# Kernel tuning notes

Hardware: AMD Instinct MI355X
Metric: run time of the kernel (lower is better)

Reference implementation:

```python
import jax, jax.numpy as jnp
import numpy as np

N_NODES = 50000
N_EDGES = 800000
HIDDEN = 128
MSG = 128


def setup_inputs() -> dict:
    key = jax.random.key(0)
    ks = jax.random.split(key, 10)
    s = 0.05
    return {
        "x": jax.random.normal(ks[0], (N_NODES, HIDDEN), jnp.float32),
        "h": jax.random.normal(ks[1], (N_NODES, HIDDEN), jnp.float32),
        "src": jax.random.randint(ks[2], (N_EDGES,), 0, N_NODES, jnp.int32),
        "dst": jax.random.randint(ks[3], (N_EDGES,), 0, N_NODES, jnp.int32),
        "W_msg": s * jax.random.normal(ks[4], (MSG, 2 * HIDDEN), jnp.float32),
        "b_msg": s * jax.random.normal(ks[5], (MSG,), jnp.float32),
        "W_ih": s * jax.random.normal(ks[6], (3 * HIDDEN, HIDDEN + MSG), jnp.float32),
        "W_hh": s * jax.random.normal(ks[7], (3 * HIDDEN, HIDDEN), jnp.float32),
        "b_ih": s * jax.random.normal(ks[8], (3 * HIDDEN,), jnp.float32),
        "b_hh": s * jax.random.normal(ks[9], (3 * HIDDEN,), jnp.float32),
    }


def reference(x, h, src, dst, W_msg, b_msg, W_ih, W_hh, b_ih, b_hh):
    N = x.shape[0]
    # --- message: linear on concat(x_src, detached h_src) -> [E, MSG]
    h_det = jax.lax.stop_gradient(h)  # h.detach() in original
    feat = jnp.concatenate([x[src], h_det[src]], axis=1)  # [E, 2H]
    m = feat @ W_msg.T + b_msg  # [E, MSG]
    # --- mean aggregation over incoming edges; isolated nodes get zeros (DGL semantics)
    msum = jax.ops.segment_sum(m, dst, num_segments=N)  # [N, MSG]
    deg = jax.ops.segment_sum(jnp.ones((src.shape[0],), m.dtype), dst, num_segments=N)
    c = msum / jnp.maximum(deg, 1.0)[:, None]
    # --- GRUCell update (PyTorch GRUCell math)
    inp = jnp.concatenate([x, c], axis=1)  # [N, H+MSG]
    gi = inp @ W_ih.T + b_ih
    gh = h @ W_hh.T + b_hh
    i_r, i_z, i_n = jnp.split(gi, 3, axis=1)
    h_r, h_z, h_n = jnp.split(gh, 3, axis=1)
    r = jax.nn.sigmoid(i_r + h_r)
    z = jax.nn.sigmoid(i_z + h_z)
    n = jnp.tanh(i_n + r * h_n)
    return (1.0 - z) * n + z * h
```

## Files before the change

### kernel.cpp

```cpp
#include <hip/hip_runtime.h>

#define H 128
#define CAP 5120

typedef __attribute__((ext_vector_type(8))) short s16x8;
typedef __attribute__((ext_vector_type(2))) float f32x2;
typedef __attribute__((ext_vector_type(4))) float f32x4;

#define WAITBAR(N) asm volatile("s_waitcnt vmcnt(" #N ")\n\ts_barrier" ::: "memory")
#define BARO() asm volatile("s_barrier" ::: "memory")

__device__ __forceinline__ float bf2f(unsigned short u){
  unsigned x = ((unsigned)u) << 16;
  return __builtin_bit_cast(float, x);
}
__device__ __forceinline__ unsigned short f2bf(float f){
  unsigned u = __builtin_bit_cast(unsigned, f);
  u += 0x7fff + ((u >> 16) & 1);
  return (unsigned short)(u >> 16);
}

typedef __attribute__((address_space(1))) void gvoid;
typedef __attribute__((address_space(3))) void lvoid;
__device__ __forceinline__ void gload16(const void* g, void* l){
  __builtin_amdgcn_global_load_lds((gvoid*)(void*)g, (lvoid*)l, 16, 0, 0);
}

__global__ void pcfs_kernel(const float* x_, const float* h, const int* src, const int* dst,
                            const float* W_msg, const float* W_ih, const float* W_hh,
                            const float* b_ih, const float* b_hh,
                            unsigned short* xhs, unsigned char* xq,
                            unsigned* bucketArr, int* bucketCnt,
                            unsigned short* WmsgT, unsigned short* WbigT, float* biasb,
                            int NB, int YE, int nv, int E){
  int blk = blockIdx.x, tid = threadIdx.x;
  if(blk < YE){
    __shared__ int hcnt[256];
    __shared__ int hpos[256];
    hcnt[tid] = 0;
    __syncthreads();
    int base = blk*2048;
    unsigned pk[8]; int bk[8];
    #pragma unroll
    for(int it=0; it<8; ++it){
      int e = base + it*256 + tid;
      bk[it] = -1;
      if(e < E){
        int d = dst[e], s = src[e];
        pk[it] = ((unsigned)d << 16) | (unsigned)s;
        int b = d >> 8;
        bk[it] = b;
        atomicAdd(&hcnt[b], 1);
      }
    }
    __syncthreads();
    if(tid < NB){
      int c = hcnt[tid];
      hpos[tid] = (c > 0) ? atomicAdd(&bucketCnt[tid*32], c) : 0;
    }
    __syncthreads();
    #pragma unroll
    for(int it=0; it<8; ++it){
      if(bk[it] >= 0){
        int p = atomicAdd(&hpos[bk[it]], 1);
        if(p < CAP) bucketArr[(long)bk[it]*CAP + p] = pk[it];
      }
    }
    return;
  }
  long w0 = (long)(blk - YE)*2048 + tid;
  const int NW = 512*384;
  #pragma unroll 1
  for(int it=0; it<8; ++it){
    long w = w0 + (long)it*256;
    if(w < 2L*nv){
      const float* sp; long j; int add;
      if(w < nv){ sp = x_; j = w; add = 0; }
      else { sp = h; j = w - nv; add = 128; }
      float4 v = ((const float4*)sp)[j];
      ushort4 o; o.x=f2bf(v.x); o.y=f2bf(v.y); o.z=f2bf(v.z); o.w=f2bf(v.w);
      int node = (int)(j >> 5), col = add + ((int)j & 31)*4;
      int k = col >> 5, wc = col & 31;
      *(ushort4*)(xhs + (long)k*nv + node*32 + wc) = o;
      int r = __builtin_amdgcn_cvt_pk_fp8_f32(v.x, v.y, 0, false);
      r = __builtin_amdgcn_cvt_pk_fp8_f32(v.z, v.w, r, true);
      *(unsigned int*)(xq + (long)k*nv + node*32 + wc) = (unsigned)r;
      continue;
    }
    long i = w - 2L*nv;
    if(i < NW){
      int hf = (int)(i / 98304); int r1 = (int)(i % 98304);
      int kt = r1 / 16384; int r2 = r1 % 16384;
      int row = r2 / 64;   int r3 = r2 % 64;
      int cw = r3 >> 3;    int j = r3 & 7;
      int c = cw ^ (row & 7);
      int k = kt*64 + c*8 + j;
      int rp = hf*256 + row;
      int q = rp >> 2, g = rp & 3;
      float v;
      if(g < 3){
        int orow = g*128 + q;
        v = (k < 256) ? W_ih[orow*256 + k] : W_hh[orow*128 + (k-256)];
      } else {
        v = (k < 256) ? 0.f : W_hh[(256 + q)*128 + (k-256)];
      }
      WbigT[i] = f2bf(v);
    } else if(i < NW + 128*256){
      int j2 = (int)(i - NW);
      int kt = j2 / 8192; int r2 = j2 % 8192;
      int row = r2 / 64;  int r3 = r2 % 64;
      int cw = r3 >> 3;   int j = r3 & 7;
      int c = cw ^ (row & 7);
      int k = kt*64 + c*8 + j;
      WmsgT[j2] = f2bf(W_msg[row*256 + k]);
    } else if(i < NW + 128*256 + 512){
      int r = (int)(i - NW - 128*256);
      int q = r >> 2, g = r & 3;
      biasb[r] = (g < 3) ? (b_ih[g*128+q] + b_hh[g*128+q]) : b_hh[256+q];
    }
  }
}

__global__ void fill2_kernel(const unsigned* bucketArr, const int* bucketCnt,
                             int* rc, unsigned short* ss16, int N){
  __shared__ int lcnt[256];
  int b = blockIdx.x, tid = threadIdx.x;
  lcnt[tid] = 0;
  __syncthreads();
  int cnt = bucketCnt[b*32]; if(cnt > CAP) cnt = CAP;
  int nbase = b << 8;
  const unsigned* arr = bucketArr + (long)b*CAP;
  for(int i = tid; i < cnt; i += 256){
    unsigned e = arr[i];
    int d = e >> 16, s = e & 0xffff;
    int p = atomicAdd(&lcnt[d - nbase], 1);
    if(p < 128) ss16[((long)d << 7) + p] = (unsigned short)s;
  }
  __syncthreads();
  int node = nbase + tid;
  if(node < N) rc[node] = lcnt[tid];
}

__global__ void agg_kernel(const unsigned char* xq, const int* rc, const unsigned short* ss16,
                           unsigned short* Sb, int N){
  int tid = threadIdx.x;
  int group = tid >> 2, sub = tid & 3;
  int node = blockIdx.y*64 + group;
  if(node >= N) return;
  const unsigned char* base = xq + (long)blockIdx.x*(long)N*32;
  int cnt = rc[node];
  int use = (cnt < 128) ? cnt : 128;
  const long e0 = (long)node << 7;
  int co = sub*8;
  float a[8] = {0.f,0.f,0.f,0.f,0.f,0.f,0.f,0.f};
  int i = 0;
  for(; i+3 < use; i += 4){
    ushort4 idx = *(const ushort4*)(ss16 + e0 + i);
    uint2 q0 = *(const uint2*)(base + (long)idx.x*32 + co);
    uint2 q1 = *(const uint2*)(base + (long)idx.y*32 + co);
    uint2 q2 = *(const uint2*)(base + (long)idx.z*32 + co);
    uint2 q3 = *(const uint2*)(base + (long)idx.w*32 + co);
    #define ACC8(q) { \
      f32x2 l0 = __builtin_amdgcn_cvt_pk_f32_fp8((q).x, false); \
      f32x2 h0 = __builtin_amdgcn_cvt_pk_f32_fp8((q).x, true);  \
      f32x2 l1 = __builtin_amdgcn_cvt_pk_f32_fp8((q).y, false); \
      f32x2 h1 = __builtin_amdgcn_cvt_pk_f32_fp8((q).y, true);  \
      a[0]+=l0[0]; a[1]+=l0[1]; a[2]+=h0[0]; a[3]+=h0[1]; \
      a[4]+=l1[0]; a[5]+=l1[1]; a[6]+=h1[0]; a[7]+=h1[1]; }
    ACC8(q0); ACC8(q1); ACC8(q2); ACC8(q3);
  }
  for(; i < use; ++i){
    int s0 = ss16[e0 + i];
    uint2 q0 = *(const uint2*)(base + (long)s0*32 + co);
    ACC8(q0);
  }
  #undef ACC8
  float inv = (cnt > 0) ? 1.0f/(float)cnt : 0.f;
  unsigned short o[8];
  #pragma unroll
  for(int j=0;j<8;++j) o[j] = f2bf(a[j]*inv);
  *(s16x8*)(Sb + (long)node*256 + blockIdx.x*32 + co) = *(const s16x8*)o;
}

__global__ __launch_bounds__(512, 2) void fused_kernel(
    const unsigned short* xhs, const unsigned short* Sb,
    const unsigned short* WmsgT, const unsigned short* WbigT,
    const float* b_msg, const float* biasb, const int* deg,
    float* outp, int NN){
  __shared__ __align__(16) char lds[131072];
  char* W0 = lds;
  char* W1 = lds + 32768;
  char* N0 = lds + 65536;
  char* N1 = lds + 81920;
  char* ldsC = lds + 98304;
  float* ldsO = (float*)(lds + 32768);

  int tid = threadIdx.x;
  int lane = tid & 63, wv = tid >> 6;
  int l15 = lane & 15, l4 = lane >> 4;
  long nodebase = (long)blockIdx.x * 128;
  const long NV = (long)NN * 32;
  const f32x4 fz = {0.f,0.f,0.f,0.f};

  auto stageS = [&](int koff, char* dst){
    #pragma unroll
    for(int it=0; it<2; ++it){
      int slot = it*512 + tid;
      int row = slot >> 3, cw = slot & 7;
      int c = cw ^ (row & 7);
      long gr = nodebase + row; if(gr > NN-1) gr = NN-1;
      gload16(Sb + gr*256 + koff + c*8, dst + it*8192 + wv*1024);
    }
  };
  auto stageX = [&](int koff, char* dst){
    #pragma unroll
    for(int it=0; it<2; ++it){
      int slot = it*512 + tid;
      int row = slot >> 3, cw = slot & 7;
      int c = cw ^ (row & 7);
      int col = koff + c*8;
      int k = col >> 5, wc = col & 31;
      long gr = nodebase + row; if(gr > NN-1) gr = NN-1;
      gload16(xhs + (long)k*NV + gr*32 + wc, dst + it*8192 + wv*1024);
    }
  };
  auto stageW1k = [&](int kt, char* dst){
    #pragma unroll
    for(int it=0; it<2; ++it){
      int slot = it*512 + tid;
      gload16(WmsgT + kt*8192 + slot*8, dst + it*8192 + wv*1024);
    }
  };
  auto stageW3k = [&](int idx, char* dst){
    #pragma unroll
    for(int it=0; it<4; ++it){
      int slot = it*512 + tid;
      gload16(WbigT + (long)idx*16384 + slot*8, dst + it*8192 + wv*1024);
    }
  };

  int wm1 = wv >> 2, wn1 = wv & 3;
  f32x4 acc1[4][2];
  #pragma unroll
  for(int m=0;m<4;++m){ acc1[m][0]=fz; acc1[m][1]=fz; }

  auto compute1 = [&](const char* Wb, const char* Nb){
    __builtin_amdgcn_s_setprio(1);
    #pragma unroll
    for(int kk=0; kk<2; ++kk){
      s16x8 af[4], bn[2];
      #pragma unroll
      for(int m=0;m<4;++m){
        int fr = wm1*64 + m*16 + l15;
        af[m] = *(const s16x8*)(Wb + fr*128 + (((kk*4+l4) ^ (fr&7))*16));
      }
      #pragma unroll
      for(int n=0;n<2;++n){
        int nr = wn1*32 + n*16 + l15;
        bn[n] = *(const s16x8*)(Nb + nr*128 + (((kk*4+l4) ^ (nr&7))*16));
      }
      #pragma unroll
      for(int m=0;m<4;++m)
        #pragma unroll
        for(int n=0;n<2;++n)
          acc1[m][n] = __builtin_amdgcn_mfma_f32_16x16x32_bf16(af[m], bn[n], acc1[m][n], 0, 0, 0);
    }
    __builtin_amdgcn_s_setprio(0);
  };

  stageW1k(0, W0); stageS(0, N0);
  stageW1k(1, W1); stageS(64, N1);
  WAITBAR(4); compute1(W0, N0); BARO();
  stageW1k(2, W0); stageS(128, N0);
  WAITBAR(4); compute1(W1, N1); BARO();
  stageW1k(3, W1); stageS(192, N1);
  WAITBAR(4); compute1(W0, N0); BARO();
  stageW3k(0, W0); stageX(0, N0);
  WAITBAR(6); compute1(W1, N1); BARO();

  #pragma unroll
  for(int n=0;n<2;++n){
    int node_l = wn1*32 + n*16 + l15;
    long gn = nodebase + node_l; if(gn > NN-1) gn = NN-1;
    int dg = deg[gn];
    float msk = (dg > 0) ? 1.f : 0.f;
    #pragma unroll
    for(int m=0;m<4;++m){
      int ccb = wm1*64 + m*16 + l4*4;
      float4 bm = *(const float4*)(b_msg + ccb);
      ushort4 o;
      o.x = f2bf((acc1[m][n][0] + bm.x)*msk);
      o.y = f2bf((acc1[m][n][1] + bm.y)*msk);
      o.z = f2bf((acc1[m][n][2] + bm.z)*msk);
      o.w = f2bf((acc1[m][n][3] + bm.w)*msk);
      *(ushort4*)(ldsC + node_l*256 + (((ccb>>3) ^ (node_l&7))*16) + (ccb&4)*2) = o;
    }
  }
  __syncthreads();

  int wm = wv >> 1, wn = wv & 1;

  auto runHalf = [&](int hf){
    f32x4 acc3[4][4];
    #pragma unroll
    for(int m=0;m<4;++m)
      #pragma unroll
      for(int n=0;n<4;++n) acc3[m][n] = fz;

    auto computeN = [&](const char* Wb, const char* Nb){
      __builtin_amdgcn_s_setprio(1);
      #pragma unroll
      for(int kk=0; kk<2; ++kk){
        s16x8 af[4], bn[4];
        #pragma unroll
        for(int m=0;m<4;++m){
          int fr = wm*64 + m*16 + l15;
          af[m] = *(const s16x8*)(Wb + fr*128 + (((kk*4+l4) ^ (fr&7))*16));
        }
        #pragma unroll
        for(int n=0;n<4;++n){
          int nr = wn*64 + n*16 + l15;
          bn[n] = *(const s16x8*)(Nb + nr*128 + (((kk*4+l4) ^ (nr&7))*16));
        }
        #pragma unroll
        for(int m=0;m<4;++m)
          #pragma unroll
          for(int n=0;n<4;++n)
            acc3[m][n] = __builtin_amdgcn_mfma_f32_16x16x32_bf16(af[m], bn[n], acc3[m][n], 0, 0, 0);
      }
      __builtin_amdgcn_s_setprio(0);
    };
    auto computeC = [&](const char* Wb, int ktc){
      __builtin_amdgcn_s_setprio(1);
      #pragma unroll
      for(int kk=0; kk<2; ++kk){
        s16x8 af[4], bn[4];
        #pragma unroll
        for(int m=0;m<4;++m){
          int fr = wm*64 + m*16 + l15;
          af[m] = *(const s16x8*)(Wb + fr*128 + (((kk*4+l4) ^ (fr&7))*16));
        }
        #pragma unroll
        for(int n=0;n<4;++n){
          int nr = wn*64 + n*16 + l15;
          bn[n] = *(const s16x8*)(ldsC + nr*256 + (((ktc*8 + kk*4 + l4) ^ (nr&7))*16));
        }
        #pragma unroll
        for(int m=0;m<4;++m)
          #pragma unroll
          for(int n=0;n<4;++n)
            acc3[m][n] = __builtin_amdgcn_mfma_f32_16x16x32_bf16(af[m], bn[n], acc3[m][n], 0, 0, 0);
      }
      __builtin_amdgcn_s_setprio(0);
    };

    if(hf == 1) stageX(0, N0);
    stageW3k(hf*6+1, W1); stageX(64, N1);
    WAITBAR(6); computeN(W0, N0); BARO();
    stageW3k(hf*6+2, W0);
    WAITBAR(4); computeN(W1, N1); BARO();
    stageW3k(hf*6+3, W1);
    WAITBAR(4); computeC(W0, 0); BARO();
    stageW3k(hf*6+4, W0); stageX(128, N0);
    WAITBAR(6); computeC(W1, 1); BARO();
    stageW3k(hf*6+5, W1); stageX(192, N1);
    WAITBAR(6); computeN(W0, N0); BARO();
    if(hf == 0){
      stageW3k(6, W0);
      WAITBAR(4); computeN(W1, N1); BARO();
    } else {
      WAITBAR(0); computeN(W1, N1); BARO();
    }

    const char* hbuf = (hf == 0) ? N0 : N1;
    #pragma unroll
    for(int m=0;m<4;++m){
      int q = hf*64 + wm*16 + m*4 + l4;
      int ql = q & 63;
      float4 bb = *(const float4*)(biasb + q*4);
      #pragma unroll
      for(int n=0;n<4;++n){
        int node_l = wn*64 + n*16 + l15;
        unsigned short hu = *(const unsigned short*)(hbuf + node_l*128 +
                              (((ql>>3) ^ (node_l&7))*16) + (ql&7)*2);
        float hv = bf2f(hu);
        float vr  = acc3[m][n][0] + bb.x;
        float vz  = acc3[m][n][1] + bb.y;
        float vsn = acc3[m][n][2] + bb.z;
        float vhn = acc3[m][n][3] + bb.w;
        float r = 1.f/(1.f + __expf(-vr));
        float z = 1.f/(1.f + __expf(-vz));
        float narg = vsn + (r - 1.f)*vhn;
        float nn2 = 2.f/(1.f + __expf(-2.f*narg)) - 1.f;
        ldsO[node_l*64 + ql] = (1.f - z)*nn2 + z*hv;
      }
    }
    __syncthreads();

    #pragma unroll
    for(int it=0; it<4; ++it){
      int slot = it*512 + tid;
      int node_l = slot >> 4, f4 = slot & 15;
      long gn = nodebase + node_l;
      if(gn < NN){
        float4 v = *(const float4*)(ldsO + node_l*64 + f4*4);
        *(float4*)(outp + gn*128 + hf*64 + f4*4) = v;
      }
    }
    __syncthreads();
  };

  runHalf(0);
  runHalf(1);
}

extern "C" void kernel_launch(void* const* d_in, const int* in_sizes, int n_in,
                              void* d_out, int out_size, void* d_ws, size_t ws_size,
                              hipStream_t stream){
  const float* x     = (const float*)d_in[0];
  const float* h     = (const float*)d_in[1];
  const int*   src   = (const int*)d_in[2];
  const int*   dst   = (const int*)d_in[3];
  const float* W_msg = (const float*)d_in[4];
  const float* b_msg = (const float*)d_in[5];
  const float* W_ih  = (const float*)d_in[6];
  const float* W_hh  = (const float*)d_in[7];
  const float* b_ih  = (const float*)d_in[8];
  const float* b_hh  = (const float*)d_in[9];
  const int N = in_sizes[0] / H;
  const int E = in_sizes[2];
  float* out = (float*)d_out;

  char* p = (char*)d_ws;
  auto alloc = [&](size_t bytes)->char*{
    char* r = p; p += (bytes + 255) & ~(size_t)255; return r;
  };
  unsigned short* xhs   = (unsigned short*)alloc((size_t)N*256*2);
  unsigned short* Sb    = (unsigned short*)alloc((size_t)N*256*2);
  unsigned char*  xq    = (unsigned char*)alloc((size_t)N*256);
  unsigned short* WmsgT = (unsigned short*)alloc(128*256*2);
  unsigned short* WbigT = (unsigned short*)alloc(512*384*2);
  float*          biasb = (float*)alloc(512*4);
  int*            rc    = (int*)alloc((size_t)N*4);
  unsigned short* ss16  = (unsigned short*)alloc((size_t)N*128*2);
  int NB = (N + 255) >> 8;
  unsigned*       bktA  = (unsigned*)alloc((size_t)NB*CAP*4);
  int*            bktC  = (int*)alloc((size_t)NB*32*4);

  hipMemsetAsync(bktC, 0, (size_t)NB*32*4, stream);
  int nv = N*H/4;
  const int NPREP = 512*384 + 128*256 + 512;
  int YE = (E + 2047)/2048;
  long convTotal = 2L*nv + NPREP;
  int YC = (int)((convTotal + 2047)/2048);
  pcfs_kernel<<<YE + YC, 256, 0, stream>>>(
      x, h, src, dst, W_msg, W_ih, W_hh, b_ih, b_hh,
      xhs, xq, bktA, bktC, WmsgT, WbigT, biasb, NB, YE, nv, E);

  fill2_kernel<<<NB, 256, 0, stream>>>(bktA, bktC, rc, ss16, N);

  dim3 gagg(8, (N + 63)/64);
  agg_kernel<<<gagg, 256, 0, stream>>>(xq, rc, ss16, Sb, N);

  int nblk = (N + 127)/128;
  fused_kernel<<<nblk, 512, 0, stream>>>(
      xhs, Sb, WmsgT, WbigT, b_msg, biasb, rc, out, N);
}
```

Before: 130.7 us.

## Fold message linear into GRU input weights, removing first GEMM stage

```diff
diff --git a/kernel.cpp b/kernel.cpp
--- a/kernel.cpp
+++ b/kernel.cpp
@@ -27,11 +27,12 @@
 }
 
 __global__ void pcfs_kernel(const float* x_, const float* h, const int* src, const int* dst,
-                            const float* W_msg, const float* W_ih, const float* W_hh,
+                            const float* W_msg, const float* b_msg,
+                            const float* W_ih, const float* W_hh,
                             const float* b_ih, const float* b_hh,
                             unsigned short* xhs, unsigned char* xq,
                             unsigned* bucketArr, int* bucketCnt,
-                            unsigned short* WmsgT, unsigned short* WbigT, float* biasb,
+                            unsigned short* WbigT, float* biasb, float* bcv,
                             int NB, int YE, int nv, int E){
   int blk = blockIdx.x, tid = threadIdx.x;
   if(blk < YE){
@@ -69,7 +70,7 @@
     return;
   }
   long w0 = (long)(blk - YE)*2048 + tid;
-  const int NW = 512*384;
+  const int NW = 512*512;
   #pragma unroll 1
   for(int it=0; it<8; ++it){
     long w = w0 + (long)it*256;
@@ -89,34 +90,43 @@
     }
     long i = w - 2L*nv;
     if(i < NW){
-      int hf = (int)(i / 98304); int r1 = (int)(i % 98304);
-      int kt = r1 / 16384; int r2 = r1 % 16384;
-      int row = r2 / 64;   int r3 = r2 % 64;
-      int cw = r3 >> 3;    int j = r3 & 7;
+      int hf = (int)(i >> 17);  int r1 = (int)(i & 131071);
+      int kt = r1 >> 14;        int r2 = r1 & 16383;
+      int row = r2 >> 6;        int r3 = r2 & 63;
+      int cw = r3 >> 3;         int j = r3 & 7;
       int c = cw ^ (row & 7);
       int k = kt*64 + c*8 + j;
       int rp = hf*256 + row;
       int q = rp >> 2, g = rp & 3;
       float v;
+      if(g == 3){
+        v = (k >= 384) ? W_hh[(256+q)*128 + (k-384)] : 0.f;
+      } else {
+        int orow = g*128 + q;
+        if(k < 128) v = W_ih[orow*256 + k];
+        else if(k < 384){
+          int s = k - 128;
+          float acc = 0.f;
+          for(int m2 = 0; m2 < 128; ++m2)
+            acc += W_ih[orow*256 + 128 + m2] * W_msg[m2*256 + s];
+          v = acc;
+        } else v = W_hh[orow*128 + (k-384)];
+      }
+      WbigT[i] = f2bf(v);
+    } else if(i < NW + 512){
+      int r = (int)(i - NW);
+      int q = r >> 2, g = r & 3;
+      biasb[r] = (g < 3) ? (b_ih[g*128+q] + b_hh[g*128+q]) : b_hh[256+q];
+    } else if(i < NW + 1024){
+      int r = (int)(i - NW - 512);
+      int q = r >> 2, g = r & 3;
+      float acc = 0.f;
       if(g < 3){
         int orow = g*128 + q;
-        v = (k < 256) ? W_ih[orow*256 + k] : W_hh[orow*128 + (k-256)];
-      } else {
-        v = (k < 256) ? 0.f : W_hh[(256 + q)*128 + (k-256)];
-      }
-      WbigT[i] = f2bf(v);
-    } else if(i < NW + 128*256){
-      int j2 = (int)(i - NW);
-      int kt = j2 / 8192; int r2 = j2 % 8192;
-      int row = r2 / 64;  int r3 = r2 % 64;
-      int cw = r3 >> 3;   int j = r3 & 7;
-      int c = cw ^ (row & 7);
-      int k = kt*64 + c*8 + j;
-      WmsgT[j2] = f2bf(W_msg[row*256 + k]);
-    } else if(i < NW + 128*256 + 512){
-      int r = (int)(i - NW - 128*256);
-      int q = r >> 2, g = r & 3;
-      biasb[r] = (g < 3) ? (b_ih[g*128+q] + b_hh[g*128+q]) : b_hh[256+q];
+        for(int m2 = 0; m2 < 128; ++m2)
+          acc += W_ih[orow*256 + 128 + m2] * b_msg[m2];
+      }
+      bcv[r] = acc;
     }
   }
 }
@@ -184,15 +194,13 @@
 
 __global__ __launch_bounds__(512, 2) void fused_kernel(
     const unsigned short* xhs, const unsigned short* Sb,
-    const unsigned short* WmsgT, const unsigned short* WbigT,
-    const float* b_msg, const float* biasb, const int* deg,
-    float* outp, int NN){
-  __shared__ __align__(16) char lds[131072];
+    const unsigned short* WbigT, const float* biasb, const float* bcv,
+    const int* deg, float* outp, int NN){
+  __shared__ __align__(16) char lds[98304];
   char* W0 = lds;
   char* W1 = lds + 32768;
   char* N0 = lds + 65536;
   char* N1 = lds + 81920;
-  char* ldsC = lds + 98304;
   float* ldsO = (float*)(lds + 32768);
 
   int tid = threadIdx.x;
@@ -224,14 +232,12 @@
       gload16(xhs + (long)k*NV + gr*32 + wc, dst + it*8192 + wv*1024);
     }
   };
-  auto stageW1k = [&](int kt, char* dst){
-    #pragma unroll
-    for(int it=0; it<2; ++it){
-      int slot = it*512 + tid;
-      gload16(WmsgT + kt*8192 + slot*8, dst + it*8192 + wv*1024);
-    }
+  auto stageK = [&](int kt, char* dst){
+    if(kt < 2) stageX(kt*64, dst);
+    else if(kt < 6) stageS((kt-2)*64, dst);
+    else stageX(128 + (kt-6)*64, dst);
   };
-  auto stageW3k = [&](int idx, char* dst){
+  auto stageW = [&](int idx, char* dst){
     #pragma unroll
     for(int it=0; it<4; ++it){
       int slot = it*512 + tid;
@@ -239,75 +245,19 @@
     }
   };
 
-  int wm1 = wv >> 2, wn1 = wv & 3;
-  f32x4 acc1[4][2];
-  #pragma unroll
-  for(int m=0;m<4;++m){ acc1[m][0]=fz; acc1[m][1]=fz; }
-
-  auto compute1 = [&](const char* Wb, const char* Nb){
-    __builtin_amdgcn_s_setprio(1);
-    #pragma unroll
-    for(int kk=0; kk<2; ++kk){
-      s16x8 af[4], bn[2];
-      #pragma unroll
-      for(int m=0;m<4;++m){
-        int fr = wm1*64 + m*16 + l15;
-        af[m] = *(const s16x8*)(Wb + fr*128 + (((kk*4+l4) ^ (fr&7))*16));
-      }
-      #pragma unroll
-      for(int n=0;n<2;++n){
-        int nr = wn1*32 + n*16 + l15;
-        bn[n] = *(const s16x8*)(Nb + nr*128 + (((kk*4+l4) ^ (nr&7))*16));
-      }
-      #pragma unroll
-      for(int m=0;m<4;++m)
-        #pragma unroll
-        for(int n=0;n<2;++n)
-          acc1[m][n] = __builtin_amdgcn_mfma_f32_16x16x32_bf16(af[m], bn[n], acc1[m][n], 0, 0, 0);
-    }
-    __builtin_amdgcn_s_setprio(0);
-  };
-
-  stageW1k(0, W0); stageS(0, N0);
-  stageW1k(1, W1); stageS(64, N1);
-  WAITBAR(4); compute1(W0, N0); BARO();
-  stageW1k(2, W0); stageS(128, N0);
-  WAITBAR(4); compute1(W1, N1); BARO();
-  stageW1k(3, W1); stageS(192, N1);
-  WAITBAR(4); compute1(W0, N0); BARO();
-  stageW3k(0, W0); stageX(0, N0);
-  WAITBAR(6); compute1(W1, N1); BARO();
-
-  #pragma unroll
-  for(int n=0;n<2;++n){
-    int node_l = wn1*32 + n*16 + l15;
-    long gn = nodebase + node_l; if(gn > NN-1) gn = NN-1;
-    int dg = deg[gn];
-    float msk = (dg > 0) ? 1.f : 0.f;
-    #pragma unroll
-    for(int m=0;m<4;++m){
-      int ccb = wm1*64 + m*16 + l4*4;
-      float4 bm = *(const float4*)(b_msg + ccb);
-      ushort4 o;
-      o.x = f2bf((acc1[m][n][0] + bm.x)*msk);
-      o.y = f2bf((acc1[m][n][1] + bm.y)*msk);
-      o.z = f2bf((acc1[m][n][2] + bm.z)*msk);
-      o.w = f2bf((acc1[m][n][3] + bm.w)*msk);
-      *(ushort4*)(ldsC + node_l*256 + (((ccb>>3) ^ (node_l&7))*16) + (ccb&4)*2) = o;
-    }
-  }
-  __syncthreads();
-
   int wm = wv >> 1, wn = wv & 1;
 
-  auto runHalf = [&](int hf){
+  stageW(0, W0); stageK(0, N0);
+
+  #pragma unroll 1
+  for(int hf=0; hf<2; ++hf){
     f32x4 acc3[4][4];
     #pragma unroll
     for(int m=0;m<4;++m)
       #pragma unroll
       for(int n=0;n<4;++n) acc3[m][n] = fz;
 
-    auto computeN = [&](const char* Wb, const char* Nb){
+    auto compute = [&](const char* Wb, const char* Nb){
       __builtin_amdgcn_s_setprio(1);
       #pragma unroll
       for(int kk=0; kk<2; ++kk){
@@ -330,88 +280,70 @@
       }
       __builtin_amdgcn_s_setprio(0);
     };
-    auto computeC = [&](const char* Wb, int ktc){
-      __builtin_amdgcn_s_setprio(1);
-      #pragma unroll
-      for(int kk=0; kk<2; ++kk){
-        s16x8 af[4], bn[4];
-        #pragma unroll
-        for(int m=0;m<4;++m){
-          int fr = wm*64 + m*16 + l15;
-          af[m] = *(const s16x8*)(Wb + fr*128 + (((kk*4+l4) ^ (fr&7))*16));
-        }
-        #pragma unroll
-        for(int n=0;n<4;++n){
-          int nr = wn*64 + n*16 + l15;
-          bn[n] = *(const s16x8*)(ldsC + nr*256 + (((ktc*8 + kk*4 + l4) ^ (nr&7))*16));
-        }
-        #pragma unroll
-        for(int m=0;m<4;++m)
-          #pragma unroll
-          for(int n=0;n<4;++n)
-            acc3[m][n] = __builtin_amdgcn_mfma_f32_16x16x32_bf16(af[m], bn[n], acc3[m][n], 0, 0, 0);
-      }
-      __builtin_amdgcn_s_setprio(0);
-    };
-
-    if(hf == 1) stageX(0, N0);
-    stageW3k(hf*6+1, W1); stageX(64, N1);
-    WAITBAR(6); computeN(W0, N0); BARO();
-    stageW3k(hf*6+2, W0);
-    WAITBAR(4); computeN(W1, N1); BARO();
-    stageW3k(hf*6+3, W1);
-    WAITBAR(4); computeC(W0, 0); BARO();
-    stageW3k(hf*6+4, W0); stageX(128, N0);
-    WAITBAR(6); computeC(W1, 1); BARO();
-    stageW3k(hf*6+5, W1); stageX(192, N1);
-    WAITBAR(6); computeN(W0, N0); BARO();
-    if(hf == 0){
-      stageW3k(6, W0);
-      WAITBAR(4); computeN(W1, N1); BARO();
-    } else {
-      WAITBAR(0); computeN(W1, N1); BARO();
+
+    if(hf == 1) stageK(0, N0);
+    #pragma unroll
+    for(int kt=0; kt<8; ++kt){
+      char* cw_ = (kt&1) ? W1 : W0;
+      char* cn_ = (kt&1) ? N1 : N0;
+      char* nw_ = (kt&1) ? W0 : W1;
+      char* nn_ = (kt&1) ? N0 : N1;
+      if(kt < 7){
+        stageW(hf*8 + kt + 1, nw_); stageK(kt + 1, nn_);
+        WAITBAR(6);
+      } else if(hf == 0){
+        stageW(8, W0);
+        WAITBAR(4);
+      } else {
+        WAITBAR(0);
+      }
+      compute(cw_, cn_);
+      BARO();
     }
 
     const char* hbuf = (hf == 0) ? N0 : N1;
+    float mk[4];
+    #pragma unroll
+    for(int n=0;n<4;++n){
+      long gn = nodebase + wn*64 + n*16 + l15; if(gn > NN-1) gn = NN-1;
+      mk[n] = (deg[gn] > 0) ? 1.f : 0.f;
+    }
     #pragma unroll
     for(int m=0;m<4;++m){
       int q = hf*64 + wm*16 + m*4 + l4;
       int ql = q & 63;
-      float4 bb = *(const float4*)(biasb + q*4);
+      float4 bb  = *(const float4*)(biasb + q*4);
+      float4 bcq = *(const float4*)(bcv + q*4);
       #pragma unroll
       for(int n=0;n<4;++n){
         int node_l = wn*64 + n*16 + l15;
         unsigned short hu = *(const unsigned short*)(hbuf + node_l*128 +
                               (((ql>>3) ^ (node_l&7))*16) + (ql&7)*2);
         float hv = bf2f(hu);
-        float vr  = acc3[m][n][0] + bb.x;
-        float vz  = acc3[m][n][1] + bb.y;
-        float vsn = acc3[m][n][2] + bb.z;
-        float vhn = acc3[m][n][3] + bb.w;
+        float vr  = acc3[m][n][0] + bb.x + mk[n]*bcq.x;
+        float vz  = acc3[m][n][1] + bb.y + mk[n]*bcq.y;
+        float vsn = acc3[m][n][2] + bb.z + mk[n]*bcq.z;
+        float vhn = acc3[m][n][3] + bb.w + mk[n]*bcq.w;
         float r = 1.f/(1.f + __expf(-vr));
         float z = 1.f/(1.f + __expf(-vz));
         float narg = vsn + (r - 1.f)*vhn;
         float nn2 = 2.f/(1.f + __expf(-2.f*narg)) - 1.f;
-        ldsO[node_l*64 + ql] = (1.f - z)*nn2 + z*hv;
+        ldsO[node_l*64 + (ql ^ ((node_l & 15) << 2))] = (1.f - z)*nn2 + z*hv;
       }
     }
     __syncthreads();
-
     #pragma unroll
     for(int it=0; it<4; ++it){
       int slot = it*512 + tid;
       int node_l = slot >> 4, f4 = slot & 15;
       long gn = nodebase + node_l;
       if(gn < NN){
-        float4 v = *(const float4*)(ldsO + node_l*64 + f4*4);
+        float4 v = *(const float4*)(ldsO + node_l*64 + (((f4*4) ^ ((node_l & 15) << 2))));
         *(float4*)(outp + gn*128 + hf*64 + f4*4) = v;
       }
     }
     __syncthreads();
-  };
-
-  runHalf(0);
-  runHalf(1);
+  }
 }
 
 extern "C" void kernel_launch(void* const* d_in, const int* in_sizes, int n_in,
@@ -438,9 +370,9 @@
   unsigned short* xhs   = (unsigned short*)alloc((size_t)N*256*2);
   unsigned short* Sb    = (unsigned short*)alloc((size_t)N*256*2);
   unsigned char*  xq    = (unsigned char*)alloc((size_t)N*256);
-  unsigned short* WmsgT = (unsigned short*)alloc(128*256*2);
-  unsigned short* WbigT = (unsigned short*)alloc(512*384*2);
+  unsigned short* WbigT = (unsigned short*)alloc(512*512*2);
   float*          biasb = (float*)alloc(512*4);
+  float*          bcv   = (float*)alloc(512*4);
   int*            rc    = (int*)alloc((size_t)N*4);
   unsigned short* ss16  = (unsigned short*)alloc((size_t)N*128*2);
   int NB = (N + 255) >> 8;
@@ -449,13 +381,13 @@
 
   hipMemsetAsync(bktC, 0, (size_t)NB*32*4, stream);
   int nv = N*H/4;
-  const int NPREP = 512*384 + 128*256 + 512;
+  const int NPREP = 512*512 + 1024;
   int YE = (E + 2047)/2048;
   long convTotal = 2L*nv + NPREP;
   int YC = (int)((convTotal + 2047)/2048);
   pcfs_kernel<<<YE + YC, 256, 0, stream>>>(
-      x, h, src, dst, W_msg, W_ih, W_hh, b_ih, b_hh,
-      xhs, xq, bktA, bktC, WmsgT, WbigT, biasb, NB, YE, nv, E);
+      x, h, src, dst, W_msg, b_msg, W_ih, W_hh, b_ih, b_hh,
+      xhs, xq, bktA, bktC, WbigT, biasb, bcv, NB, YE, nv, E);
 
   fill2_kernel<<<NB, 256, 0, stream>>>(bktA, bktC, rc, ss16, N);
 
@@ -464,5 +396,5 @@
 
   int nblk = (N + 127)/128;
   fused_kernel<<<nblk, 512, 0, stream>>>(
-      xhs, Sb, WmsgT, WbigT, b_msg, biasb, rc, out, N);
-}
+      xhs, Sb, WbigT, biasb, bcv, rc, out, N);
+}
```

Measured after the change: 158.9 us. 21.6% more time.
